# Kernel optimization log

Measured on AMD Instinct MI355X. Metric: run time of the kernel, lower is better.

Reference implementation:

```python
import jax, jax.numpy as jnp
import numpy as np

N_EMBD = 1024
N_HEAD = 16
HEAD_DIM = N_EMBD // N_HEAD


def setup_inputs() -> dict:
    key = jax.random.key(0)
    k1, k2, k3 = jax.random.split(key, 3)
    x = jax.random.normal(k1, (2, 2048, N_EMBD), dtype=jnp.float32)
    # torch Linear weight shapes: c_attn [3*n_embd, n_embd], c_proj [n_embd, n_embd]
    w_attn = jax.random.normal(k2, (3 * N_EMBD, N_EMBD), dtype=jnp.float32) * 0.02
    w_proj = jax.random.normal(k3, (N_EMBD, N_EMBD), dtype=jnp.float32) * 0.02
    return {"x": x, "w_attn": w_attn, "w_proj": w_proj}


def reference(x, w_attn, w_proj):
    B, T, C = x.shape
    qkv = x @ w_attn.T  # [B,T,3C]
    q, k, v = jnp.split(qkv, 3, axis=2)
    # [B,T,H,D] -> [B,H,T,D]
    def heads(t):
        return t.reshape(B, T, N_HEAD, HEAD_DIM).transpose(0, 2, 1, 3)
    q, k, v = heads(q), heads(k), heads(v)
    scale = 1.0 / jnp.sqrt(jnp.asarray(HEAD_DIM, dtype=x.dtype))
    att = jnp.einsum('bhqd,bhkd->bhqk', q, k) * scale
    causal = jnp.tril(jnp.ones((T, T), dtype=bool))
    att = jnp.where(causal[None, None], att, jnp.asarray(-jnp.inf, dtype=att.dtype))
    att = jax.nn.softmax(att, axis=-1)
    y = jnp.einsum('bhqk,bhkd->bhqd', att, v)
    y = y.transpose(0, 2, 1, 3).reshape(B, T, C)
    return y @ w_proj.T
```

## Files before the change

kernel.cpp:

```cpp
#include <hip/hip_runtime.h>

#define BSZ 2
#define SEQ 2048
#define NEMBD 1024
#define NHEAD 16
#define HDIM 64
#define BT (BSZ * SEQ)
#define QKV_LD (3 * NEMBD)
#define SCALE_LOG2E 0.1803368665f

typedef unsigned short u16;
typedef __attribute__((ext_vector_type(8))) short short8;
typedef __attribute__((ext_vector_type(4))) float floatx4;
typedef __attribute__((ext_vector_type(4))) unsigned short ushort4v;

#define MFMA16(a, b, c) __builtin_amdgcn_mfma_f32_16x16x32_bf16(a, b, c, 0, 0, 0)

__device__ __forceinline__ void gload_lds16(const void* g, void* l) {
  __builtin_amdgcn_global_load_lds(
      (const __attribute__((address_space(1))) unsigned int*)(g),
      (__attribute__((address_space(3))) unsigned int*)(l), 16, 0, 0);
}

__device__ __forceinline__ u16 f2bf(float f) {
  unsigned int u = __builtin_bit_cast(unsigned int, f);
  u += 0x7FFFu + ((u >> 16) & 1u);
  return (u16)(u >> 16);
}

__device__ __forceinline__ float bf2f(u16 v) {
  return __builtin_bit_cast(float, (unsigned)v << 16);
}

#define N_X  (BT * NEMBD)
#define N_WA (QKV_LD * NEMBD)
#define N_WP (NEMBD * NEMBD)
__global__ __launch_bounds__(256) void cvt_all(const float* __restrict__ x,
                                               const float* __restrict__ wa,
                                               const float* __restrict__ wp,
                                               u16* __restrict__ xb,
                                               u16* __restrict__ wab,
                                               u16* __restrict__ wpb) {
  int i = (blockIdx.x * 256 + threadIdx.x) * 8;
  const float* src;
  u16* dst;
  if (i < N_X)            { src = x + i;              dst = xb + i; }
  else if (i < N_X + N_WA){ src = wa + (i - N_X);     dst = wab + (i - N_X); }
  else                    { src = wp + (i - N_X - N_WA); dst = wpb + (i - N_X - N_WA); }
  float4 a = *(const float4*)(src);
  float4 b = *(const float4*)(src + 4);
  short8 o;
  o[0] = (short)f2bf(a.x); o[1] = (short)f2bf(a.y);
  o[2] = (short)f2bf(a.z); o[3] = (short)f2bf(a.w);
  o[4] = (short)f2bf(b.x); o[5] = (short)f2bf(b.y);
  o[6] = (short)f2bf(b.z); o[7] = (short)f2bf(b.w);
  *(short8*)(dst) = o;
}

__global__ __launch_bounds__(256) void gemm_qkv(const u16* __restrict__ A,
                                                const u16* __restrict__ B,
                                                u16* __restrict__ qkb,
                                                u16* __restrict__ vtg) {
  __shared__ __align__(16) u16 As[128 * 64];
  __shared__ __align__(16) u16 Bs[128 * 64];
  const int t = threadIdx.x;
  const int lane = t & 63, w = t >> 6;
  const int l15 = lane & 15, quad = lane >> 4;
  const int wm = w >> 1, wn = w & 1;
  const int m0 = blockIdx.y * 128, n0 = blockIdx.x * 128;
  const int is_v = (n0 >= 2 * NEMBD);

  const int srow8 = t >> 3;
  const int kc = (t & 7) ^ (srow8 & 7);
  const u16* gA = A + (size_t)(m0 + srow8) * NEMBD + kc * 8;
  const u16* gB = B + (size_t)(n0 + srow8) * NEMBD + kc * 8;

  floatx4 acc[4][4] = {};
  short8 ra[4], rb[4];

#define QKV_LOAD(K0)                                                           \
  { _Pragma("unroll")                                                          \
    for (int is = 0; is < 4; ++is) {                                           \
      ra[is] = *(const short8*)(gA + (size_t)(is * 32) * NEMBD + (K0));        \
      rb[is] = *(const short8*)(gB + (size_t)(is * 32) * NEMBD + (K0));        \
    } }
#define QKV_WRITE()                                                            \
  { _Pragma("unroll")                                                          \
    for (int is = 0; is < 4; ++is) {                                           \
      *(short8*)&As[(is * 256 + t) * 8] = ra[is];                              \
      *(short8*)&Bs[(is * 256 + t) * 8] = rb[is];                              \
    } }

  QKV_LOAD(0);
  QKV_WRITE();
  __syncthreads();

  for (int k0 = 0; k0 < NEMBD; k0 += 64) {
    const int more = (k0 + 64 < NEMBD);
    if (more) QKV_LOAD(k0 + 64);
#pragma unroll
    for (int kh = 0; kh < 2; ++kh) {
      short8 af[4], bfr[4];
#pragma unroll
      for (int mt = 0; mt < 4; ++mt) {
        int row = wm * 64 + mt * 16 + l15;
        af[mt] = *(const short8*)&As[row * 64 + (((kh * 4 + quad) ^ (row & 7)) * 8)];
      }
#pragma unroll
      for (int nt = 0; nt < 4; ++nt) {
        int row = wn * 64 + nt * 16 + l15;
        bfr[nt] = *(const short8*)&Bs[row * 64 + (((kh * 4 + quad) ^ (row & 7)) * 8)];
      }
      if (is_v) {
#pragma unroll
        for (int mt = 0; mt < 4; ++mt)
#pragma unroll
          for (int nt = 0; nt < 4; ++nt)
            acc[mt][nt] = MFMA16(af[mt], bfr[nt], acc[mt][nt]);
      } else {
#pragma unroll
        for (int mt = 0; mt < 4; ++mt)
#pragma unroll
          for (int nt = 0; nt < 4; ++nt)
            acc[mt][nt] = MFMA16(bfr[nt], af[mt], acc[mt][nt]);
      }
    }
    __syncthreads();
    if (more) {
      QKV_WRITE();
      __syncthreads();
    }
  }
#undef QKV_LOAD
#undef QKV_WRITE

  if (is_v) {
#pragma unroll
    for (int mt = 0; mt < 4; ++mt)
#pragma unroll
      for (int nt = 0; nt < 4; ++nt) {
        int hd = n0 + wn * 64 + nt * 16 + l15 - 2 * NEMBD;
        int token = m0 + wm * 64 + mt * 16 + quad * 4;
        int b = token >> 11, tp = token & (SEQ - 1);
        ushort4v pk;
#pragma unroll
        for (int r = 0; r < 4; ++r) pk[r] = f2bf(acc[mt][nt][r]);
        *(ushort4v*)&vtg[((size_t)(b * NEMBD + hd)) * SEQ + tp] = pk;
      }
  } else {
#pragma unroll
    for (int mt = 0; mt < 4; ++mt) {
      size_t token = (size_t)(m0 + wm * 64 + mt * 16 + l15);
#pragma unroll
      for (int nt = 0; nt < 4; ++nt) {
        int nc = n0 + wn * 64 + nt * 16 + quad * 4;
        ushort4v pk;
#pragma unroll
        for (int r = 0; r < 4; ++r) pk[r] = f2bf(acc[mt][nt][r]);
        *(ushort4v*)&qkb[token * 2048 + nc] = pk;
      }
    }
  }
}

__global__ __launch_bounds__(256) void attn_mfma4(const u16* __restrict__ qkb,
                                                  const u16* __restrict__ vtg,
                                                  u16* __restrict__ opart,
                                                  float* __restrict__ lpart) {
  const int bx = blockIdx.x;
  const int qt = 15 - (bx >> 6);
  const int r6 = bx & 63;
  const int bh = r6 >> 1, half = r6 & 1;
  const int b = bh >> 4, h = bh & 15;
  const int t = threadIdx.x, lane = t & 63, w = t >> 6;
  const int l15 = lane & 15, quad = lane >> 4;

  __shared__ __align__(16) u16 S[25600];
  u16* Qs  = S;
  u16* KV0 = S + 8192;
  u16* KV1 = S;
  u16* Pa  = S + 16384;

  const int kt0 = half ? (qt + 1) : 0;
  const int nkt = qt + 1;

  {
    const u16* qb = qkb + ((size_t)(b * SEQ + qt * 128)) * 2048 + h * HDIM;
#pragma unroll
    for (int is = 0; is < 4; ++is) {
      int s = is * 256 + t;
      int row = s >> 3, pos = s & 7;
      int kc = pos ^ (row & 7);
      gload_lds16(qb + (size_t)row * 2048 + kc * 8, &Qs[s * 8]);
    }
  }

#define STAGE_KV(KT, BUF)                                                      \
  {                                                                            \
    const u16* kb_ = qkb + ((size_t)(b * SEQ + (KT) * 64)) * 2048 + NEMBD + h * HDIM; \
    const u16* vb_ = vtg + ((size_t)(bh * 64)) * SEQ + (KT) * 64;              \
    _Pragma("unroll")                                                          \
    for (int is = 0; is < 2; ++is) {                                           \
      int s = is * 256 + t;                                                    \
      int row = s >> 3, pos = s & 7;                                           \
      int kc = pos ^ (row & 7);                                                \
      gload_lds16(kb_ + (size_t)row * 2048 + kc * 8, &(BUF)[s * 8]);           \
      gload_lds16(vb_ + (size_t)row * SEQ + kc * 8, &(BUF)[4096 + s * 8]);     \
    }                                                                          \
  }

  STAGE_KV(kt0, KV0);
  __syncthreads();

  short8 qf[2][2];
#pragma unroll
  for (int qs = 0; qs < 2; ++qs) {
    int qrow = w * 32 + qs * 16 + l15;
#pragma unroll
    for (int hf = 0; hf < 2; ++hf)
      qf[qs][hf] = *(const short8*)&Qs[qrow * 64 + (((hf * 4 + quad) ^ (qrow & 7)) * 8)];
  }
  __syncthreads();

  float rs[2] = {0.f, 0.f};
  floatx4 o_acc[2][4] = {};

#define COMPUTE_TILE(BUF, KT, MASKED)                                          \
  {                                                                            \
    floatx4 sacc[2][4];                                                        \
    _Pragma("unroll")                                                          \
    for (int nt = 0; nt < 4; ++nt) {                                           \
      int krow = nt * 16 + l15;                                                \
      short8 kf0 = *(const short8*)&(BUF)[krow * 64 + ((quad ^ (krow & 7)) * 8)]; \
      short8 kf1 = *(const short8*)&(BUF)[krow * 64 + (((4 + quad) ^ (krow & 7)) * 8)]; \
      _Pragma("unroll")                                                        \
      for (int qs = 0; qs < 2; ++qs) {                                         \
        floatx4 z = {0.f, 0.f, 0.f, 0.f};                                      \
        z = MFMA16(kf0, qf[qs][0], z);                                         \
        z = MFMA16(kf1, qf[qs][1], z);                                         \
        sacc[qs][nt] = z;                                                      \
      }                                                                        \
    }                                                                          \
    _Pragma("unroll")                                                          \
    for (int qs = 0; qs < 2; ++qs) {                                           \
      const int qg = qt * 128 + w * 32 + qs * 16 + l15;                        \
      const int kb0 = (KT) * 64 + quad * 4;                                    \
      _Pragma("unroll")                                                        \
      for (int nt = 0; nt < 4; ++nt) {                                         \
        ushort4v pk;                                                           \
        _Pragma("unroll")                                                      \
        for (int r = 0; r < 4; ++r) {                                          \
          float p = exp2f(fmaf(sacc[qs][nt][r], SCALE_LOG2E, -8.0f));          \
          if (MASKED && (kb0 + nt * 16 + r) > qg) p = 0.0f;                    \
          rs[qs] += p;                                                         \
          pk[r] = f2bf(p);                                                     \
        }                                                                      \
        *(ushort4v*)&Pa[(w * 32 + qs * 16 + l15) * 72 + nt * 16 + quad * 4] = pk; \
      }                                                                        \
    }                                                                          \
    short8 pf[2][2];                                                           \
    _Pragma("unroll")                                                          \
    for (int qs = 0; qs < 2; ++qs) {                                           \
      const int prow = w * 32 + qs * 16 + l15;                                 \
      pf[qs][0] = *(const short8*)&Pa[prow * 72 + quad * 8];                   \
      pf[qs][1] = *(const short8*)&Pa[prow * 72 + 32 + quad * 8];              \
    }                                                                          \
    _Pragma("unroll")                                                          \
    for (int nt = 0; nt < 4; ++nt) {                                           \
      int drow = nt * 16 + l15;                                                \
      short8 vf0 = *(const short8*)&(BUF)[4096 + drow * 64 + ((quad ^ (drow & 7)) * 8)]; \
      short8 vf1 = *(const short8*)&(BUF)[4096 + drow * 64 + (((4 + quad) ^ (drow & 7)) * 8)]; \
      _Pragma("unroll")                                                        \
      for (int qs = 0; qs < 2; ++qs) {                                         \
        o_acc[qs][nt] = MFMA16(pf[qs][0], vf0, o_acc[qs][nt]);                 \
        o_acc[qs][nt] = MFMA16(pf[qs][1], vf1, o_acc[qs][nt]);                 \
      }                                                                        \
    }                                                                          \
  }

  for (int i = 0; i < nkt; ++i) {
    const int kt = kt0 + i;
    u16* cur = (i & 1) ? KV1 : KV0;
    u16* nxt = (i & 1) ? KV0 : KV1;
    if (i + 1 < nkt) STAGE_KV(kt0 + i + 1, nxt);
    if (kt >= 2 * qt) { COMPUTE_TILE(cur, kt, 1); }
    else              { COMPUTE_TILE(cur, kt, 0); }
    __syncthreads();
  }
#undef COMPUTE_TILE
#undef STAGE_KV

#pragma unroll
  for (int qs = 0; qs < 2; ++qs) {
    rs[qs] += __shfl_xor(rs[qs], 16, 64);
    rs[qs] += __shfl_xor(rs[qs], 32, 64);
    if (quad == 0)
      lpart[((size_t)half * 32 + bh) * SEQ + qt * 128 + w * 32 + qs * 16 + l15] = rs[qs];
  }
  u16* ob = opart + (size_t)half * BT * NEMBD;
#pragma unroll
  for (int qs = 0; qs < 2; ++qs)
#pragma unroll
    for (int nt = 0; nt < 4; ++nt)
#pragma unroll
      for (int r = 0; r < 4; ++r) {
        size_t tok = (size_t)(b * SEQ + qt * 128 + w * 32 + qs * 16 + quad * 4 + r);
        ob[tok * NEMBD + h * HDIM + nt * 16 + l15] = f2bf(o_acc[qs][nt][r]);
      }
}

__global__ __launch_bounds__(256) void combine(const u16* __restrict__ opart,
                                               const float* __restrict__ lpart,
                                               u16* __restrict__ yb) {
  int idx = (blockIdx.x * 256 + threadIdx.x) * 4;
  int tok = idx >> 10, c = idx & 1023;
  int b = tok >> 11, q = tok & (SEQ - 1), h = c >> 6;
  float l = lpart[(size_t)(b * 16 + h) * SEQ + q] +
            lpart[(size_t)(32 + b * 16 + h) * SEQ + q];
  float inv = 1.0f / l;
  ushort4v o0 = *(const ushort4v*)&opart[idx];
  ushort4v o1 = *(const ushort4v*)&opart[(size_t)BT * NEMBD + idx];
  ushort4v yo;
#pragma unroll
  for (int j = 0; j < 4; ++j) {
    float f0 = bf2f(o0[j]);
    float f1 = bf2f(o1[j]);
    yo[j] = f2bf((f0 + f1) * inv);
  }
  *(ushort4v*)&yb[idx] = yo;
}

__global__ __launch_bounds__(256) void gemm_out(const u16* __restrict__ A,
                                                const u16* __restrict__ B,
                                                float* __restrict__ C) {
  __shared__ __align__(16) u16 S[2][12288];
  const int t = threadIdx.x;
  const int lane = t & 63, w = t >> 6;
  const int l15 = lane & 15, quad = lane >> 4;
  const int wm = w >> 1, wn = w & 1;
  const int m0 = blockIdx.y * 128, n0 = blockIdx.x * 64;

  const int srow8 = t >> 3;
  const int kc = (t & 7) ^ (srow8 & 7);

#define OUT_STAGE(K0, BUF)                                                     \
  { u16* as_ = &S[BUF][0]; u16* bs_ = &S[BUF][8192];                           \
    _Pragma("unroll")                                                          \
    for (int is = 0; is < 4; ++is)                                             \
      gload_lds16(A + (size_t)(m0 + is * 32 + srow8) * NEMBD + (K0) + kc * 8,  \
                  &as_[(is * 256 + t) * 8]);                                   \
    _Pragma("unroll")                                                          \
    for (int is = 0; is < 2; ++is)                                             \
      gload_lds16(B + (size_t)(n0 + is * 32 + srow8) * NEMBD + (K0) + kc * 8,  \
                  &bs_[(is * 256 + t) * 8]); }

  floatx4 acc[4][2] = {};

  OUT_STAGE(0, 0);
  __syncthreads();

  int ib = 0;
  for (int k0 = 0; k0 < NEMBD; k0 += 64, ib ^= 1) {
    if (k0 + 64 < NEMBD) OUT_STAGE(k0 + 64, ib ^ 1);
    const u16* as_ = &S[ib][0];
    const u16* bs_ = &S[ib][8192];
#pragma unroll
    for (int kh = 0; kh < 2; ++kh) {
      short8 af[4], bfr[2];
#pragma unroll
      for (int mt = 0; mt < 4; ++mt) {
        int row = wm * 64 + mt * 16 + l15;
        af[mt] = *(const short8*)&as_[row * 64 + (((kh * 4 + quad) ^ (row & 7)) * 8)];
      }
#pragma unroll
      for (int nt = 0; nt < 2; ++nt) {
        int row = wn * 32 + nt * 16 + l15;
        bfr[nt] = *(const short8*)&bs_[row * 64 + (((kh * 4 + quad) ^ (row & 7)) * 8)];
      }
#pragma unroll
      for (int mt = 0; mt < 4; ++mt)
#pragma unroll
        for (int nt = 0; nt < 2; ++nt)
          acc[mt][nt] = MFMA16(bfr[nt], af[mt], acc[mt][nt]);
    }
    __syncthreads();
  }
#undef OUT_STAGE

#pragma unroll
  for (int mt = 0; mt < 4; ++mt) {
    size_t token = (size_t)(m0 + wm * 64 + mt * 16 + l15);
#pragma unroll
    for (int nt = 0; nt < 2; ++nt) {
      int nc = n0 + wn * 32 + nt * 16 + quad * 4;
      float4 v = make_float4(acc[mt][nt][0], acc[mt][nt][1],
                             acc[mt][nt][2], acc[mt][nt][3]);
      *(float4*)&C[token * NEMBD + nc] = v;
    }
  }
}

extern "C" void kernel_launch(void* const* d_in, const int* in_sizes, int n_in,
                              void* d_out, int out_size, void* d_ws, size_t ws_size,
                              hipStream_t stream) {
  const float* x      = (const float*)d_in[0];
  const float* w_attn = (const float*)d_in[1];
  const float* w_proj = (const float*)d_in[2];
  float* out = (float*)d_out;

  u16* base  = (u16*)d_ws;
  u16* opart = base;
  u16* xb    = base;
  u16* wab   = base + 4194304;
  u16* wpb   = base + 8388608;
  u16* qkb   = base + 9437184;
  u16* vtg   = base + 17825792;
  u16* yb    = base + 22020096;
  float* lpart = (float*)(base + 26214400);

  cvt_all<<<(N_X + N_WA + N_WP) / 2048, 256, 0, stream>>>(x, w_attn, w_proj, xb, wab, wpb);

  gemm_qkv<<<dim3(QKV_LD / 128, BT / 128), 256, 0, stream>>>(xb, wab, qkb, vtg);

  attn_mfma4<<<dim3((SEQ / 128) * BSZ * NHEAD * 2), 256, 0, stream>>>(qkb, vtg, opart, lpart);

  combine<<<(BT * NEMBD) / 1024, 256, 0, stream>>>(opart, lpart, yb);

  gemm_out<<<dim3(NEMBD / 64, BT / 128), 256, 0, stream>>>(yb, wpb, out);
}
```

Measured before the change: 187.6 us.

## Fuse x conversion into QKV GEMM and split-combine into output GEMM

Drops the separate fp32-to-bf16 conversion of x and converts it while staging each tile of the QKV GEMM. The combine kernel is removed: the output projection GEMM now loads both attention partials and their row sums, normalizes and rounds to bf16 as it writes the A tile to shared memory. This saves two launches and the intermediate writes and reads of xb and yb. In exchange, gemm_qkv reads twice the A bytes per tile, and gemm_out loses its double-buffered async LDS loads for register staging with an extra barrier. The x tiles are also converted again by every column block.

```diff
diff --git a/kernel.cpp b/kernel.cpp
--- a/kernel.cpp
+++ b/kernel.cpp
@@ -32,21 +32,17 @@
   return __builtin_bit_cast(float, (unsigned)v << 16);
 }
 
-#define N_X  (BT * NEMBD)
 #define N_WA (QKV_LD * NEMBD)
 #define N_WP (NEMBD * NEMBD)
-__global__ __launch_bounds__(256) void cvt_all(const float* __restrict__ x,
-                                               const float* __restrict__ wa,
-                                               const float* __restrict__ wp,
-                                               u16* __restrict__ xb,
-                                               u16* __restrict__ wab,
-                                               u16* __restrict__ wpb) {
+__global__ __launch_bounds__(256) void cvt_w(const float* __restrict__ wa,
+                                             const float* __restrict__ wp,
+                                             u16* __restrict__ wab,
+                                             u16* __restrict__ wpb) {
   int i = (blockIdx.x * 256 + threadIdx.x) * 8;
   const float* src;
   u16* dst;
-  if (i < N_X)            { src = x + i;              dst = xb + i; }
-  else if (i < N_X + N_WA){ src = wa + (i - N_X);     dst = wab + (i - N_X); }
-  else                    { src = wp + (i - N_X - N_WA); dst = wpb + (i - N_X - N_WA); }
+  if (i < N_WA) { src = wa + i;          dst = wab + i; }
+  else          { src = wp + (i - N_WA); dst = wpb + (i - N_WA); }
   float4 a = *(const float4*)(src);
   float4 b = *(const float4*)(src + 4);
   short8 o;
@@ -57,7 +53,7 @@
   *(short8*)(dst) = o;
 }
 
-__global__ __launch_bounds__(256) void gemm_qkv(const u16* __restrict__ A,
+__global__ __launch_bounds__(256) void gemm_qkv(const float* __restrict__ X,
                                                 const u16* __restrict__ B,
                                                 u16* __restrict__ qkb,
                                                 u16* __restrict__ vtg) {
@@ -72,22 +68,29 @@
 
   const int srow8 = t >> 3;
   const int kc = (t & 7) ^ (srow8 & 7);
-  const u16* gA = A + (size_t)(m0 + srow8) * NEMBD + kc * 8;
-  const u16* gB = B + (size_t)(n0 + srow8) * NEMBD + kc * 8;
+  const float* gA = X + (size_t)(m0 + srow8) * NEMBD + kc * 8;
+  const u16*   gB = B + (size_t)(n0 + srow8) * NEMBD + kc * 8;
 
   floatx4 acc[4][4] = {};
-  short8 ra[4], rb[4];
+  float4 rax[4][2];
+  short8 rb[4];
 
 #define QKV_LOAD(K0)                                                           \
   { _Pragma("unroll")                                                          \
     for (int is = 0; is < 4; ++is) {                                           \
-      ra[is] = *(const short8*)(gA + (size_t)(is * 32) * NEMBD + (K0));        \
-      rb[is] = *(const short8*)(gB + (size_t)(is * 32) * NEMBD + (K0));        \
+      rax[is][0] = *(const float4*)(gA + (size_t)(is * 32) * NEMBD + (K0));    \
+      rax[is][1] = *(const float4*)(gA + (size_t)(is * 32) * NEMBD + (K0) + 4);\
+      rb[is]     = *(const short8*)(gB + (size_t)(is * 32) * NEMBD + (K0));    \
     } }
 #define QKV_WRITE()                                                            \
   { _Pragma("unroll")                                                          \
     for (int is = 0; is < 4; ++is) {                                           \
-      *(short8*)&As[(is * 256 + t) * 8] = ra[is];                              \
+      short8 v;                                                                \
+      v[0] = (short)f2bf(rax[is][0].x); v[1] = (short)f2bf(rax[is][0].y);      \
+      v[2] = (short)f2bf(rax[is][0].z); v[3] = (short)f2bf(rax[is][0].w);      \
+      v[4] = (short)f2bf(rax[is][1].x); v[5] = (short)f2bf(rax[is][1].y);      \
+      v[6] = (short)f2bf(rax[is][1].z); v[7] = (short)f2bf(rax[is][1].w);      \
+      *(short8*)&As[(is * 256 + t) * 8] = v;                                   \
       *(short8*)&Bs[(is * 256 + t) * 8] = rb[is];                              \
     } }
 
@@ -309,31 +312,12 @@
       }
 }
 
-__global__ __launch_bounds__(256) void combine(const u16* __restrict__ opart,
-                                               const float* __restrict__ lpart,
-                                               u16* __restrict__ yb) {
-  int idx = (blockIdx.x * 256 + threadIdx.x) * 4;
-  int tok = idx >> 10, c = idx & 1023;
-  int b = tok >> 11, q = tok & (SEQ - 1), h = c >> 6;
-  float l = lpart[(size_t)(b * 16 + h) * SEQ + q] +
-            lpart[(size_t)(32 + b * 16 + h) * SEQ + q];
-  float inv = 1.0f / l;
-  ushort4v o0 = *(const ushort4v*)&opart[idx];
-  ushort4v o1 = *(const ushort4v*)&opart[(size_t)BT * NEMBD + idx];
-  ushort4v yo;
-#pragma unroll
-  for (int j = 0; j < 4; ++j) {
-    float f0 = bf2f(o0[j]);
-    float f1 = bf2f(o1[j]);
-    yo[j] = f2bf((f0 + f1) * inv);
-  }
-  *(ushort4v*)&yb[idx] = yo;
-}
-
-__global__ __launch_bounds__(256) void gemm_out(const u16* __restrict__ A,
+__global__ __launch_bounds__(256) void gemm_out(const u16* __restrict__ opart,
+                                                const float* __restrict__ lpart,
                                                 const u16* __restrict__ B,
                                                 float* __restrict__ C) {
-  __shared__ __align__(16) u16 S[2][12288];
+  __shared__ __align__(16) u16 As[128 * 64];
+  __shared__ __align__(16) u16 Bs[64 * 64];
   const int t = threadIdx.x;
   const int lane = t & 63, w = t >> 6;
   const int l15 = lane & 15, quad = lane >> 4;
@@ -342,40 +326,61 @@
 
   const int srow8 = t >> 3;
   const int kc = (t & 7) ^ (srow8 & 7);
-
-#define OUT_STAGE(K0, BUF)                                                     \
-  { u16* as_ = &S[BUF][0]; u16* bs_ = &S[BUF][8192];                           \
-    _Pragma("unroll")                                                          \
-    for (int is = 0; is < 4; ++is)                                             \
-      gload_lds16(A + (size_t)(m0 + is * 32 + srow8) * NEMBD + (K0) + kc * 8,  \
-                  &as_[(is * 256 + t) * 8]);                                   \
+  const u16* gO0 = opart + (size_t)(m0 + srow8) * NEMBD + kc * 8;
+  const u16* gO1 = gO0 + (size_t)BT * NEMBD;
+  const u16* gB  = B + (size_t)(n0 + srow8) * NEMBD + kc * 8;
+  const int tokb = (m0 + srow8) >> 11;
+  const int tokq0 = (m0 + srow8) & (SEQ - 1);
+
+  floatx4 acc[4][2] = {};
+  short8 ro0[4], ro1[4], rb[2];
+  float rl0[4], rl1[4];
+
+#define OUT_LOAD(K0)                                                           \
+  { const int h_ = (K0) >> 6;                                                  \
+    _Pragma("unroll")                                                          \
+    for (int is = 0; is < 4; ++is) {                                           \
+      ro0[is] = *(const short8*)(gO0 + (size_t)(is * 32) * NEMBD + (K0));      \
+      ro1[is] = *(const short8*)(gO1 + (size_t)(is * 32) * NEMBD + (K0));      \
+      rl0[is] = lpart[(size_t)(tokb * 16 + h_) * SEQ + tokq0 + is * 32];       \
+      rl1[is] = lpart[(size_t)(32 + tokb * 16 + h_) * SEQ + tokq0 + is * 32];  \
+    }                                                                          \
     _Pragma("unroll")                                                          \
     for (int is = 0; is < 2; ++is)                                             \
-      gload_lds16(B + (size_t)(n0 + is * 32 + srow8) * NEMBD + (K0) + kc * 8,  \
-                  &bs_[(is * 256 + t) * 8]); }
-
-  floatx4 acc[4][2] = {};
-
-  OUT_STAGE(0, 0);
+      rb[is] = *(const short8*)(gB + (size_t)(is * 32) * NEMBD + (K0)); }
+#define OUT_WRITE()                                                            \
+  { _Pragma("unroll")                                                          \
+    for (int is = 0; is < 4; ++is) {                                           \
+      float inv = 1.0f / (rl0[is] + rl1[is]);                                  \
+      short8 v;                                                                \
+      _Pragma("unroll")                                                        \
+      for (int j = 0; j < 8; ++j)                                              \
+        v[j] = (short)f2bf((bf2f((u16)ro0[is][j]) + bf2f((u16)ro1[is][j])) * inv); \
+      *(short8*)&As[(is * 256 + t) * 8] = v;                                   \
+    }                                                                          \
+    _Pragma("unroll")                                                          \
+    for (int is = 0; is < 2; ++is)                                             \
+      *(short8*)&Bs[(is * 256 + t) * 8] = rb[is]; }
+
+  OUT_LOAD(0);
+  OUT_WRITE();
   __syncthreads();
 
-  int ib = 0;
-  for (int k0 = 0; k0 < NEMBD; k0 += 64, ib ^= 1) {
-    if (k0 + 64 < NEMBD) OUT_STAGE(k0 + 64, ib ^ 1);
-    const u16* as_ = &S[ib][0];
-    const u16* bs_ = &S[ib][8192];
+  for (int k0 = 0; k0 < NEMBD; k0 += 64) {
+    const int more = (k0 + 64 < NEMBD);
+    if (more) OUT_LOAD(k0 + 64);
 #pragma unroll
     for (int kh = 0; kh < 2; ++kh) {
       short8 af[4], bfr[2];
 #pragma unroll
       for (int mt = 0; mt < 4; ++mt) {
         int row = wm * 64 + mt * 16 + l15;
-        af[mt] = *(const short8*)&as_[row * 64 + (((kh * 4 + quad) ^ (row & 7)) * 8)];
+        af[mt] = *(const short8*)&As[row * 64 + (((kh * 4 + quad) ^ (row & 7)) * 8)];
       }
 #pragma unroll
       for (int nt = 0; nt < 2; ++nt) {
         int row = wn * 32 + nt * 16 + l15;
-        bfr[nt] = *(const short8*)&bs_[row * 64 + (((kh * 4 + quad) ^ (row & 7)) * 8)];
+        bfr[nt] = *(const short8*)&Bs[row * 64 + (((kh * 4 + quad) ^ (row & 7)) * 8)];
       }
 #pragma unroll
       for (int mt = 0; mt < 4; ++mt)
@@ -384,8 +389,13 @@
           acc[mt][nt] = MFMA16(bfr[nt], af[mt], acc[mt][nt]);
     }
     __syncthreads();
-  }
-#undef OUT_STAGE
+    if (more) {
+      OUT_WRITE();
+      __syncthreads();
+    }
+  }
+#undef OUT_LOAD
+#undef OUT_WRITE
 
 #pragma unroll
   for (int mt = 0; mt < 4; ++mt) {
@@ -410,21 +420,17 @@
 
   u16* base  = (u16*)d_ws;
   u16* opart = base;
-  u16* xb    = base;
-  u16* wab   = base + 4194304;
-  u16* wpb   = base + 8388608;
-  u16* qkb   = base + 9437184;
-  u16* vtg   = base + 17825792;
-  u16* yb    = base + 22020096;
-  float* lpart = (float*)(base + 26214400);
-
-  cvt_all<<<(N_X + N_WA + N_WP) / 2048, 256, 0, stream>>>(x, w_attn, w_proj, xb, wab, wpb);
-
-  gemm_qkv<<<dim3(QKV_LD / 128, BT / 128), 256, 0, stream>>>(xb, wab, qkb, vtg);
+  u16* wab   = base + 8388608;
+  u16* wpb   = base + 11534336;
+  u16* qkb   = base + 12582912;
+  u16* vtg   = base + 20971520;
+  float* lpart = (float*)(base + 25165824);
+
+  cvt_w<<<(N_WA + N_WP) / 2048, 256, 0, stream>>>(w_attn, w_proj, wab, wpb);
+
+  gemm_qkv<<<dim3(QKV_LD / 128, BT / 128), 256, 0, stream>>>(x, wab, qkb, vtg);
 
   attn_mfma4<<<dim3((SEQ / 128) * BSZ * NHEAD * 2), 256, 0, stream>>>(qkb, vtg, opart, lpart);
 
-  combine<<<(BT * NEMBD) / 1024, 256, 0, stream>>>(opart, lpart, yb);
-
-  gemm_out<<<dim3(NEMBD / 64, BT / 128), 256, 0, stream>>>(yb, wpb, out);
-}
+  gemm_out<<<dim3(NEMBD / 64, BT / 128), 256, 0, stream>>>(opart, lpart, wpb, out);
+}
```

New measurement: 214.1 us. 14.1% more time.
